# Kernel optimization log

Measured on AMD Instinct MI355X. Metric: run time of the kernel, lower is better.

The kernel has to match this reference:

```python
import jax, jax.numpy as jnp
import numpy as np
import math

B, S, D, H, F = 2, 2048, 1024, 16, 4096
HD = D // H

def _xavier(key, fan_in, fan_out):
    limit = math.sqrt(6.0 / (fan_in + fan_out))
    return jax.random.uniform(key, (fan_in, fan_out), jnp.float32, -limit, limit)

def setup_inputs() -> dict:
    key = jax.random.key(0)
    ks = jax.random.split(key, 8)
    inp = {
        'x': jax.random.normal(ks[0], (B, S, D), jnp.float32),
        # attention projections (stored [in, out]; biases zero-init per module)
        'Wq': _xavier(ks[1], D, D), 'bq': jnp.zeros((D,), jnp.float32),
        'Wk': _xavier(ks[2], D, D), 'bk': jnp.zeros((D,), jnp.float32),
        'Wv': _xavier(ks[3], D, D), 'bv': jnp.zeros((D,), jnp.float32),
        'Wp': _xavier(ks[4], D, D), 'bp': jnp.zeros((D,), jnp.float32),
        # layer norms
        'g1': jnp.ones((D,), jnp.float32), 'be1': jnp.zeros((D,), jnp.float32),
        'g2': jnp.ones((D,), jnp.float32), 'be2': jnp.zeros((D,), jnp.float32),
        # feed-forward
        'W1': _xavier(ks[5], D, F), 'bf1': jnp.zeros((F,), jnp.float32),
        'W2': _xavier(ks[6], F, D), 'bf2': jnp.zeros((D,), jnp.float32),
    }
    return inp

def _layernorm(x, g, b, eps=1e-5):
    mu = jnp.mean(x, axis=-1, keepdims=True)
    var = jnp.var(x, axis=-1, keepdims=True)
    return (x - mu) * jax.lax.rsqrt(var + eps) * g + b

def _block(x, Wq, bq, Wk, bk, Wv, bv, Wp, bp, g1, be1, g2, be2, W1, bf1, W2, bf2):
    b, s, d = x.shape
    # --- pre-LN attention ---
    a_in = _layernorm(x, g1, be1)
    q = (a_in @ Wq + bq).reshape(b, s, H, HD).transpose(0, 2, 1, 3)  # [B,H,S,HD]
    k = (a_in @ Wk + bk).reshape(b, s, H, HD).transpose(0, 2, 1, 3)
    v = (a_in @ Wv + bv).reshape(b, s, H, HD).transpose(0, 2, 1, 3)
    scores = jnp.einsum('bhqd,bhkd->bhqk', q, k) / math.sqrt(HD)
    causal = jnp.tril(jnp.ones((s, s), dtype=bool))
    scores = jnp.where(causal, scores, -jnp.inf)
    attn = jax.nn.softmax(scores, axis=-1)
    out = jnp.einsum('bhqk,bhkd->bhqd', attn, v)
    out = out.transpose(0, 2, 1, 3).reshape(b, s, d)
    x = x + (out @ Wp + bp)
    # --- pre-LN feed-forward ---
    f_in = _layernorm(x, g2, be2)
    h = jax.nn.gelu(f_in @ W1 + bf1, approximate=False)
    x = x + (h @ W2 + bf2)
    return x

def reference(x, Wq, bq, Wk, bk, Wv, bv, Wp, bp, g1, be1, g2, be2, W1, bf1, W2, bf2):
    return _block(x, Wq, bq, Wk, bk, Wv, bv, Wp, bp, g1, be1, g2, be2, W1, bf1, W2, bf2)
```

## Files before the change

### kernel.cpp

```cpp
#include <hip/hip_runtime.h>
#include <hip/hip_bf16.h>

#define AS1 __attribute__((address_space(1)))
#define AS3 __attribute__((address_space(3)))

typedef __bf16 bf16;
typedef __attribute__((ext_vector_type(8))) __bf16 bf16x8;
typedef __attribute__((ext_vector_type(4))) __bf16 bf16x4;
typedef __attribute__((ext_vector_type(4))) float f32x4;

#define NB 2
#define NS 2048
#define ND 1024
#define NH 16
#define NF 4096
#define NHD 64
#define NM (NB*NS)

__device__ __forceinline__ void gload16(const void* g, void* l) {
  __builtin_amdgcn_global_load_lds((AS1 void*)g, (AS3 void*)l, 16, 0, 0);
}

__global__ void tb_wtrans(const float* __restrict__ W, bf16* __restrict__ Wt,
                          int K, int N) {
  __shared__ float t[64][65];
  const int nb = blockIdx.x << 6, kb = blockIdx.y << 6;
  const int tid = threadIdx.x;
#pragma unroll
  for (int i = 0; i < 16; ++i) {
    const int lin = tid + (i << 8);
    const int r = lin >> 6, c = lin & 63;
    t[r][c] = W[(size_t)(kb + r) * N + nb + c];
  }
  __syncthreads();
#pragma unroll
  for (int i = 0; i < 16; ++i) {
    const int lin = tid + (i << 8);
    const int r = lin >> 6, c = lin & 63;
    Wt[(size_t)(nb + r) * K + kb + c] = (bf16)t[c][r];
  }
}

__global__ void tb_vtrans(const bf16* __restrict__ v, bf16* __restrict__ vt) {
  __shared__ bf16 t[64][72];
  const int bh = blockIdx.y;
  const int sb = blockIdx.x << 6;
  const int tid = threadIdx.x;
  const bf16* src = v + ((size_t)bh * NS + sb) * NHD;
  bf16* dst = vt + (size_t)bh * NHD * NS + sb;
  const int r = tid >> 3;
  const int c8 = (tid & 7) << 3;
#pragma unroll
  for (int i = 0; i < 2; ++i) {
    const int row = r + i * 32;
    const bf16x8 xv = *(const bf16x8*)(src + (size_t)row * NHD + c8);
#pragma unroll
    for (int j = 0; j < 8; ++j) t[row][c8 + j] = xv[j];
  }
  __syncthreads();
#pragma unroll
  for (int i = 0; i < 2; ++i) {
    const int row = r + i * 32;
    bf16x8 ov;
#pragma unroll
    for (int j = 0; j < 8; ++j) ov[j] = t[c8 + j][row];
    *(bf16x8*)(dst + (size_t)row * NS + c8) = ov;
  }
}

__global__ void tb_lnorm(const float* __restrict__ xin, const float* __restrict__ g,
                         const float* __restrict__ be, bf16* __restrict__ outp) {
  const int row = blockIdx.x;
  const int tid = threadIdx.x;
  const float4 v = ((const float4*)(xin + (size_t)row * ND))[tid];
  float s  = v.x + v.y + v.z + v.w;
  float ss = v.x*v.x + v.y*v.y + v.z*v.z + v.w*v.w;
#pragma unroll
  for (int off = 32; off; off >>= 1) {
    s  += __shfl_xor(s,  off, 64);
    ss += __shfl_xor(ss, off, 64);
  }
  __shared__ float red[8];
  const int lane = tid & 63, wv = tid >> 6;
  if (lane == 0) { red[wv] = s; red[4 + wv] = ss; }
  __syncthreads();
  s  = red[0] + red[1] + red[2] + red[3];
  ss = red[4] + red[5] + red[6] + red[7];
  const float mu = s * (1.0f / ND);
  const float var = ss * (1.0f / ND) - mu * mu;
  const float rstd = rsqrtf(var + 1e-5f);
  const float4 gv = ((const float4*)g)[tid];
  const float4 bv = ((const float4*)be)[tid];
  bf16x4 o;
  o[0] = (bf16)((v.x - mu) * rstd * gv.x + bv.x);
  o[1] = (bf16)((v.y - mu) * rstd * gv.y + bv.y);
  o[2] = (bf16)((v.z - mu) * rstd * gv.z + bv.z);
  o[3] = (bf16)((v.w - mu) * rstd * gv.w + bv.w);
  ((bf16x4*)(outp + (size_t)row * ND))[tid] = o;
}

template <int MODE>
__global__ void __launch_bounds__(256, 2)
tb_gemm(const bf16* __restrict__ A,
        const bf16* __restrict__ B0, const bf16* __restrict__ B1, const bf16* __restrict__ B2,
        const float* __restrict__ bias0, const float* __restrict__ bias1, const float* __restrict__ bias2,
        const float* __restrict__ resid,
        void* __restrict__ o0, void* __restrict__ o1, void* __restrict__ o2,
        int Ktot) {
  __shared__ __align__(16) bf16 As[128 * 64];
  __shared__ __align__(16) bf16 Bs[128 * 64];
  const bf16* Bt = B0; const float* bias = bias0; void* outp = o0;
  if (MODE == 0) {
    if (blockIdx.z == 1)      { Bt = B1; bias = bias1; outp = o1; }
    else if (blockIdx.z == 2) { Bt = B2; bias = bias2; outp = o2; }
  }
  const int tid = threadIdx.x;
  const int lane = tid & 63, wv = tid >> 6;
  const int wr = wv >> 1, wc = wv & 1;
  const int m0 = blockIdx.y * 128, n0 = blockIdx.x * 128;

  f32x4 acc[4][4] = {};

  const int srow = (wv << 3) + (lane >> 3);
  const int scb  = ((lane & 7) << 4);

  for (int k0 = 0; k0 < Ktot; k0 += 64) {
    __syncthreads();
#pragma unroll
    for (int i = 0; i < 4; ++i) {
      const int row = i * 32 + srow;
      const int cb = scb ^ ((row & 7) << 4);
      gload16(A  + (size_t)(m0 + row) * Ktot + k0 + (cb >> 1), (char*)As + i * 4096 + wv * 1024);
      gload16(Bt + (size_t)(n0 + row) * Ktot + k0 + (cb >> 1), (char*)Bs + i * 4096 + wv * 1024);
    }
    __syncthreads();
#pragma unroll
    for (int kk = 0; kk < 2; ++kk) {
      bf16x8 af[4], bfr[4];
#pragma unroll
      for (int mi = 0; mi < 4; ++mi) {
        const int row = wr * 64 + mi * 16 + (lane & 15);
        const int cb = (kk * 64 + ((lane >> 4) << 4)) ^ ((row & 7) << 4);
        af[mi] = *(const bf16x8*)((const char*)As + row * 128 + cb);
      }
#pragma unroll
      for (int ni = 0; ni < 4; ++ni) {
        const int row = wc * 64 + ni * 16 + (lane & 15);
        const int cb = (kk * 64 + ((lane >> 4) << 4)) ^ ((row & 7) << 4);
        bfr[ni] = *(const bf16x8*)((const char*)Bs + row * 128 + cb);
      }
#pragma unroll
      for (int mi = 0; mi < 4; ++mi)
#pragma unroll
        for (int ni = 0; ni < 4; ++ni)
          acc[mi][ni] = __builtin_amdgcn_mfma_f32_16x16x32_bf16(af[mi], bfr[ni], acc[mi][ni], 0, 0, 0);
    }
  }
#pragma unroll
  for (int mi = 0; mi < 4; ++mi) {
#pragma unroll
    for (int ni = 0; ni < 4; ++ni) {
      const int rbase = m0 + wr * 64 + mi * 16 + ((lane >> 4) << 2);
      const int gcol  = n0 + wc * 64 + ni * 16 + (lane & 15);
#pragma unroll
      for (int r = 0; r < 4; ++r) {
        const int grow = rbase + r;
        const float val = acc[mi][ni][r] + bias[gcol];
        if (MODE == 0) {
          const int b = grow >> 11, sIdx = grow & 2047;
          const int h = gcol >> 6, hd = gcol & 63;
          ((bf16*)outp)[(((size_t)(b * NH + h)) * NS + sIdx) * NHD + hd] = (bf16)val;
        } else if (MODE == 1) {
          const size_t idx = (size_t)grow * ND + gcol;
          ((float*)outp)[idx] = resid[idx] + val;
        } else {
          const float gelu = 0.5f * val * (1.0f + erff(val * 0.70710678f));
          ((bf16*)outp)[(size_t)grow * NF + gcol] = (bf16)gelu;
        }
      }
    }
  }
}

__global__ void __launch_bounds__(256, 4)
tb_attn(const bf16* __restrict__ qg, const bf16* __restrict__ kg,
        const bf16* __restrict__ vtg, bf16* __restrict__ og) {
  __shared__ __align__(16) bf16 Ks[2][64 * 64];
  __shared__ __align__(16) bf16 Vts[2][64 * 64];
  __shared__ __align__(16) bf16 Ps[4][16 * 64];
  const int bid = blockIdx.x;
  const int u = bid & 255, v = bid >> 8;
  const int bh = u & 31;
  const int s = ((u >> 5) << 2) + v;
  const int qt = (s & 1) ? (31 - (s >> 1)) : (s >> 1);
  const int tid = threadIdx.x;
  const int lane = tid & 63, wv = tid >> 6;
  const bf16* Qp  = qg  + (size_t)bh * NS * NHD;
  const bf16* Kp  = kg  + (size_t)bh * NS * NHD;
  const bf16* Vtp = vtg + (size_t)bh * NHD * NS;
  char* const Pw = (char*)&Ps[wv][0];
  const int qbase = qt * 64 + wv * 16;

  bf16x8 qa[2];
#pragma unroll
  for (int kk = 0; kk < 2; ++kk)
    qa[kk] = *(const bf16x8*)(Qp + (size_t)(qbase + (lane & 15)) * NHD
                              + kk * 32 + ((lane >> 4) << 3));

  f32x4 Of[4] = {};
  float mrow[4], lrow[4];
#pragma unroll
  for (int r = 0; r < 4; ++r) { mrow[r] = -1e30f; lrow[r] = 0.0f; }

  const int srow = (wv << 3) + (lane >> 3);
  const int scb  = (lane & 7) << 4;
  const int nkb = qt + 1;

#define STAGE_KV(buf, kbi_) do {                                               \
    _Pragma("unroll")                                                          \
    for (int i_ = 0; i_ < 2; ++i_) {                                           \
      const int row_ = i_ * 32 + srow;                                         \
      const int cb_ = scb ^ ((row_ & 7) << 4);                                 \
      gload16(Kp  + (size_t)((kbi_) * 64 + row_) * NHD + (cb_ >> 1),           \
              (char*)Ks[buf] + i_ * 4096 + wv * 1024);                         \
      gload16(Vtp + (size_t)row_ * NS + (kbi_) * 64 + (cb_ >> 1),              \
              (char*)Vts[buf] + i_ * 4096 + wv * 1024);                        \
    } } while (0)

  STAGE_KV(0, 0);
  __syncthreads();

  for (int kbi = 0; kbi < nkb; ++kbi) {
    const int cur = kbi & 1;
    if (kbi + 1 < nkb) STAGE_KV(cur ^ 1, kbi + 1);
    const bool maskedT = (kbi == qt);

    f32x4 sf[4] = {};
#pragma unroll
    for (int kk = 0; kk < 2; ++kk) {
#pragma unroll
      for (int f = 0; f < 4; ++f) {
        const int row = f * 16 + (lane & 15);
        const int cb = (kk * 64 + ((lane >> 4) << 4)) ^ ((row & 7) << 4);
        const bf16x8 kf = *(const bf16x8*)((const char*)Ks[cur] + row * 128 + cb);
        sf[f] = __builtin_amdgcn_mfma_f32_16x16x32_bf16(qa[kk], kf, sf[f], 0, 0, 0);
      }
    }

    float tmax[4];
#pragma unroll
    for (int r = 0; r < 4; ++r) tmax[r] = -1e30f;
#pragma unroll
    for (int f = 0; f < 4; ++f)
#pragma unroll
      for (int r = 0; r < 4; ++r) {
        float sv = sf[f][r] * 0.125f;
        if (maskedT) {
          const int kcol = kbi * 64 + f * 16 + (lane & 15);
          const int qrow = qbase + ((lane >> 4) << 2) + r;
          sv = (kcol <= qrow) ? sv : -1e30f;
        }
        sf[f][r] = sv;
        tmax[r] = fmaxf(tmax[r], sv);
      }
#pragma unroll
    for (int off = 8; off; off >>= 1)
#pragma unroll
      for (int r = 0; r < 4; ++r)
        tmax[r] = fmaxf(tmax[r], __shfl_xor(tmax[r], off, 64));
#pragma unroll
    for (int r = 0; r < 4; ++r) {
      const float mnew = fmaxf(mrow[r], tmax[r]);
      const float alpha = __expf(mrow[r] - mnew);
      mrow[r] = mnew;
      float ps = 0.0f;
#pragma unroll
      for (int f = 0; f < 4; ++f) {
        const float p = __expf(sf[f][r] - mnew);
        sf[f][r] = p;
        ps += p;
      }
      lrow[r] = lrow[r] * alpha + ps;
#pragma unroll
      for (int hf = 0; hf < 4; ++hf) Of[hf][r] *= alpha;
    }

#pragma unroll
    for (int f = 0; f < 4; ++f) {
      const int col = f * 16 + (lane & 15);
#pragma unroll
      for (int r = 0; r < 4; ++r) {
        const int prow = ((lane >> 4) << 2) + r;
        *(bf16*)(Pw + prow * 128 + ((col * 2) ^ ((prow & 7) << 4))) = (bf16)sf[f][r];
      }
    }

#pragma unroll
    for (int kk = 0; kk < 2; ++kk) {
      const int prow = lane & 15;
      const int pcb = (kk * 64 + ((lane >> 4) << 4)) ^ ((prow & 7) << 4);
      const bf16x8 pa = *(const bf16x8*)(Pw + prow * 128 + pcb);
#pragma unroll
      for (int hf = 0; hf < 4; ++hf) {
        const int vrow = hf * 16 + (lane & 15);
        const int vcb = (kk * 64 + ((lane >> 4) << 4)) ^ ((vrow & 7) << 4);
        const bf16x8 vbf = *(const bf16x8*)((const char*)Vts[cur] + vrow * 128 + vcb);
        Of[hf] = __builtin_amdgcn_mfma_f32_16x16x32_bf16(pa, vbf, Of[hf], 0, 0, 0);
      }
    }
    __syncthreads();
  }
#undef STAGE_KV

#pragma unroll
  for (int off = 8; off; off >>= 1)
#pragma unroll
    for (int r = 0; r < 4; ++r)
      lrow[r] += __shfl_xor(lrow[r], off, 64);
  const int b = bh >> 4, h = bh & 15;
#pragma unroll
  for (int r = 0; r < 4; ++r) {
    const float inv = 1.0f / lrow[r];
    const int q = qbase + ((lane >> 4) << 2) + r;
    bf16* dst = og + ((size_t)b * NS + q) * ND + h * NHD;
#pragma unroll
    for (int hf = 0; hf < 4; ++hf)
      dst[hf * 16 + (lane & 15)] = (bf16)(Of[hf][r] * inv);
  }
}

extern "C" void kernel_launch(void* const* d_in, const int* in_sizes, int n_in,
                              void* d_out, int out_size, void* d_ws, size_t ws_size,
                              hipStream_t stream) {
  (void)in_sizes; (void)n_in; (void)out_size; (void)ws_size;
  const float* x   = (const float*)d_in[0];
  const float* Wq  = (const float*)d_in[1];
  const float* bq  = (const float*)d_in[2];
  const float* Wk  = (const float*)d_in[3];
  const float* bk  = (const float*)d_in[4];
  const float* Wv  = (const float*)d_in[5];
  const float* bv  = (const float*)d_in[6];
  const float* Wp  = (const float*)d_in[7];
  const float* bp  = (const float*)d_in[8];
  const float* g1  = (const float*)d_in[9];
  const float* be1 = (const float*)d_in[10];
  const float* g2  = (const float*)d_in[11];
  const float* be2 = (const float*)d_in[12];
  const float* W1  = (const float*)d_in[13];
  const float* bf1 = (const float*)d_in[14];
  const float* W2  = (const float*)d_in[15];
  const float* bf2 = (const float*)d_in[16];
  float* outp = (float*)d_out;

  char* w = (char*)d_ws;
  bf16* WqT  = (bf16*)(w + (0u  << 20));
  bf16* WkT  = (bf16*)(w + (2u  << 20));
  bf16* WvT  = (bf16*)(w + (4u  << 20));
  bf16* WpT  = (bf16*)(w + (6u  << 20));
  bf16* W1T  = (bf16*)(w + (8u  << 20));
  bf16* W2T  = (bf16*)(w + (16u << 20));
  bf16* Abuf = (bf16*)(w + (24u << 20));
  bf16* vt   = (bf16*)(w + (24u << 20));
  bf16* qb   = (bf16*)(w + (32u << 20));
  bf16* kb   = (bf16*)(w + (40u << 20));
  bf16* vb   = (bf16*)(w + (48u << 20));
  bf16* ao   = (bf16*)(w + (56u << 20));
  bf16* hb   = (bf16*)(w + (32u << 20));
  float* x2  = outp;

  tb_wtrans<<<dim3(16, 16), 256, 0, stream>>>(Wq, WqT, ND, ND);
  tb_wtrans<<<dim3(16, 16), 256, 0, stream>>>(Wk, WkT, ND, ND);
  tb_wtrans<<<dim3(16, 16), 256, 0, stream>>>(Wv, WvT, ND, ND);
  tb_wtrans<<<dim3(16, 16), 256, 0, stream>>>(Wp, WpT, ND, ND);
  tb_wtrans<<<dim3(64, 16), 256, 0, stream>>>(W1, W1T, ND, NF);
  tb_wtrans<<<dim3(16, 64), 256, 0, stream>>>(W2, W2T, NF, ND);

  tb_lnorm<<<NM, 256, 0, stream>>>(x, g1, be1, Abuf);
  tb_gemm<0><<<dim3(8, 32, 3), 256, 0, stream>>>(Abuf, WqT, WkT, WvT, bq, bk, bv,
                                                 nullptr, qb, kb, vb, ND);
  tb_vtrans<<<dim3(32, 32), 256, 0, stream>>>(vb, vt);
  tb_attn<<<1024, 256, 0, stream>>>(qb, kb, vt, ao);
  tb_gemm<1><<<dim3(8, 32, 1), 256, 0, stream>>>(ao, WpT, WpT, WpT, bp, bp, bp,
                                                 x, x2, x2, x2, ND);
  tb_lnorm<<<NM, 256, 0, stream>>>(x2, g2, be2, Abuf);
  tb_gemm<2><<<dim3(32, 32, 1), 256, 0, stream>>>(Abuf, W1T, W1T, W1T, bf1, bf1, bf1,
                                                  nullptr, hb, hb, hb, ND);
  tb_gemm<1><<<dim3(8, 32, 1), 256, 0, stream>>>(hb, W2T, W2T, W2T, bf2, bf2, bf2,
                                                 x2, outp, outp, outp, NF);
}
```

Measured before the change: 280.8 us.

## Multi-buffer GEMM LDS tiles to overlap global loads with MFMA compute

Converts the GEMM main loop from single-buffered load-then-compute into a double- or triple-buffered software pipeline. Tiles for later k-steps are issued with global_load_lds while the current tile is consumed, and explicit vmcnt waits plus s_barrier replace the paired syncthreads. The QKV and FFN1 GEMMs use two buffers; the 256-block output projection and FFN2 GEMMs use three buffers with launch bounds lowered to one block per CU. This aims to hide global memory latency behind MFMA work, at the cost of more LDS per block and possibly lower occupancy.

```diff
diff --git a/kernel.cpp b/kernel.cpp
--- a/kernel.cpp
+++ b/kernel.cpp
@@ -99,16 +99,16 @@
   ((bf16x4*)(outp + (size_t)row * ND))[tid] = o;
 }
 
-template <int MODE>
-__global__ void __launch_bounds__(256, 2)
+template <int MODE, int NBUF>
+__global__ void __launch_bounds__(256, NBUF == 2 ? 2 : 1)
 tb_gemm(const bf16* __restrict__ A,
         const bf16* __restrict__ B0, const bf16* __restrict__ B1, const bf16* __restrict__ B2,
         const float* __restrict__ bias0, const float* __restrict__ bias1, const float* __restrict__ bias2,
         const float* __restrict__ resid,
         void* __restrict__ o0, void* __restrict__ o1, void* __restrict__ o2,
         int Ktot) {
-  __shared__ __align__(16) bf16 As[128 * 64];
-  __shared__ __align__(16) bf16 Bs[128 * 64];
+  __shared__ __align__(16) bf16 As[NBUF * 128 * 64];
+  __shared__ __align__(16) bf16 Bs[NBUF * 128 * 64];
   const bf16* Bt = B0; const float* bias = bias0; void* outp = o0;
   if (MODE == 0) {
     if (blockIdx.z == 1)      { Bt = B1; bias = bias1; outp = o1; }
@@ -123,17 +123,37 @@
 
   const int srow = (wv << 3) + (lane >> 3);
   const int scb  = ((lane & 7) << 4);
-
-  for (int k0 = 0; k0 < Ktot; k0 += 64) {
-    __syncthreads();
-#pragma unroll
-    for (int i = 0; i < 4; ++i) {
-      const int row = i * 32 + srow;
-      const int cb = scb ^ ((row & 7) << 4);
-      gload16(A  + (size_t)(m0 + row) * Ktot + k0 + (cb >> 1), (char*)As + i * 4096 + wv * 1024);
-      gload16(Bt + (size_t)(n0 + row) * Ktot + k0 + (cb >> 1), (char*)Bs + i * 4096 + wv * 1024);
-    }
-    __syncthreads();
+  const int NT = Ktot >> 6;
+
+#define GSTAGE(buf, t_) do {                                                   \
+    _Pragma("unroll")                                                          \
+    for (int i_ = 0; i_ < 4; ++i_) {                                           \
+      const int row_ = i_ * 32 + srow;                                         \
+      const int cb_ = scb ^ ((row_ & 7) << 4);                                 \
+      gload16(A  + (size_t)(m0 + row_) * Ktot + ((t_) << 6) + (cb_ >> 1),      \
+              (char*)As + (buf) * 16384 + i_ * 4096 + wv * 1024);              \
+      gload16(Bt + (size_t)(n0 + row_) * Ktot + ((t_) << 6) + (cb_ >> 1),      \
+              (char*)Bs + (buf) * 16384 + i_ * 4096 + wv * 1024);              \
+    } } while (0)
+
+  GSTAGE(0, 0);
+  if (NBUF == 3 && NT > 1) {
+    GSTAGE(1, 1);
+    asm volatile("s_waitcnt vmcnt(8)" ::: "memory");
+  } else {
+    asm volatile("s_waitcnt vmcnt(0)" ::: "memory");
+  }
+  __builtin_amdgcn_s_barrier();
+
+  int cur = 0;
+  for (int t = 0; t < NT; ++t) {
+    if (NBUF == 2) {
+      if (t + 1 < NT) GSTAGE(cur ^ 1, t + 1);
+    } else {
+      if (t + 2 < NT) GSTAGE((cur + 2 >= 3 ? cur - 1 : cur + 2), t + 2);
+    }
+    const char* Ab = (const char*)As + cur * 16384;
+    const char* Bb = (const char*)Bs + cur * 16384;
 #pragma unroll
     for (int kk = 0; kk < 2; ++kk) {
       bf16x8 af[4], bfr[4];
@@ -141,13 +161,13 @@
       for (int mi = 0; mi < 4; ++mi) {
         const int row = wr * 64 + mi * 16 + (lane & 15);
         const int cb = (kk * 64 + ((lane >> 4) << 4)) ^ ((row & 7) << 4);
-        af[mi] = *(const bf16x8*)((const char*)As + row * 128 + cb);
+        af[mi] = *(const bf16x8*)(Ab + row * 128 + cb);
       }
 #pragma unroll
       for (int ni = 0; ni < 4; ++ni) {
         const int row = wc * 64 + ni * 16 + (lane & 15);
         const int cb = (kk * 64 + ((lane >> 4) << 4)) ^ ((row & 7) << 4);
-        bfr[ni] = *(const bf16x8*)((const char*)Bs + row * 128 + cb);
+        bfr[ni] = *(const bf16x8*)(Bb + row * 128 + cb);
       }
 #pragma unroll
       for (int mi = 0; mi < 4; ++mi)
@@ -155,7 +175,17 @@
         for (int ni = 0; ni < 4; ++ni)
           acc[mi][ni] = __builtin_amdgcn_mfma_f32_16x16x32_bf16(af[mi], bfr[ni], acc[mi][ni], 0, 0, 0);
     }
-  }
+    if (t + 1 < NT) {
+      if (NBUF == 3 && t + 2 < NT)
+        asm volatile("s_waitcnt vmcnt(8)" ::: "memory");
+      else
+        asm volatile("s_waitcnt vmcnt(0)" ::: "memory");
+      __builtin_amdgcn_s_barrier();
+    }
+    cur = (cur + 1 == NBUF) ? 0 : cur + 1;
+  }
+#undef GSTAGE
+
 #pragma unroll
   for (int mi = 0; mi < 4; ++mi) {
 #pragma unroll
@@ -376,15 +406,15 @@
   tb_wtrans<<<dim3(16, 64), 256, 0, stream>>>(W2, W2T, NF, ND);
 
   tb_lnorm<<<NM, 256, 0, stream>>>(x, g1, be1, Abuf);
-  tb_gemm<0><<<dim3(8, 32, 3), 256, 0, stream>>>(Abuf, WqT, WkT, WvT, bq, bk, bv,
-                                                 nullptr, qb, kb, vb, ND);
+  tb_gemm<0, 2><<<dim3(8, 32, 3), 256, 0, stream>>>(Abuf, WqT, WkT, WvT, bq, bk, bv,
+                                                    nullptr, qb, kb, vb, ND);
   tb_vtrans<<<dim3(32, 32), 256, 0, stream>>>(vb, vt);
   tb_attn<<<1024, 256, 0, stream>>>(qb, kb, vt, ao);
-  tb_gemm<1><<<dim3(8, 32, 1), 256, 0, stream>>>(ao, WpT, WpT, WpT, bp, bp, bp,
-                                                 x, x2, x2, x2, ND);
+  tb_gemm<1, 3><<<dim3(8, 32, 1), 256, 0, stream>>>(ao, WpT, WpT, WpT, bp, bp, bp,
+                                                    x, x2, x2, x2, ND);
   tb_lnorm<<<NM, 256, 0, stream>>>(x2, g2, be2, Abuf);
-  tb_gemm<2><<<dim3(32, 32, 1), 256, 0, stream>>>(Abuf, W1T, W1T, W1T, bf1, bf1, bf1,
-                                                  nullptr, hb, hb, hb, ND);
-  tb_gemm<1><<<dim3(8, 32, 1), 256, 0, stream>>>(hb, W2T, W2T, W2T, bf2, bf2, bf2,
-                                                 x2, outp, outp, outp, NF);
-}
+  tb_gemm<2, 2><<<dim3(32, 32, 1), 256, 0, stream>>>(Abuf, W1T, W1T, W1T, bf1, bf1, bf1,
+                                                     nullptr, hb, hb, hb, ND);
+  tb_gemm<1, 3><<<dim3(8, 32, 1), 256, 0, stream>>>(hb, W2T, W2T, W2T, bf2, bf2, bf2,
+                                                    x2, outp, outp, outp, NF);
+}
```

Result: slower. 292.7 us (+4.3%).

## Use 64x128 double-buffered GEMM tiles for the two N=1024 residual projections

Applied to the files above, without the earlier changes.

Adds a tb_gemm64 kernel with 64-row by 128-column tiles and double-buffered LDS staging, so the next K tile loads while the current one is multiplied. It replaces the MODE 1 path for the attention output projection and the FFN down projection. Both GEMMs have N=1024, so 128x128 tiles launched only 256 blocks. The smaller M tile doubles that to 512 blocks to fill the CUs better. The cost is less operand reuse per block, and the extra LDS buffer may lower occupancy.

```diff
diff --git a/kernel.cpp b/kernel.cpp
--- a/kernel.cpp
+++ b/kernel.cpp
@@ -104,7 +104,6 @@
 tb_gemm(const bf16* __restrict__ A,
         const bf16* __restrict__ B0, const bf16* __restrict__ B1, const bf16* __restrict__ B2,
         const float* __restrict__ bias0, const float* __restrict__ bias1, const float* __restrict__ bias2,
-        const float* __restrict__ resid,
         void* __restrict__ o0, void* __restrict__ o1, void* __restrict__ o2,
         int Ktot) {
   __shared__ __align__(16) bf16 As[128 * 64];
@@ -170,13 +169,95 @@
           const int b = grow >> 11, sIdx = grow & 2047;
           const int h = gcol >> 6, hd = gcol & 63;
           ((bf16*)outp)[(((size_t)(b * NH + h)) * NS + sIdx) * NHD + hd] = (bf16)val;
-        } else if (MODE == 1) {
-          const size_t idx = (size_t)grow * ND + gcol;
-          ((float*)outp)[idx] = resid[idx] + val;
         } else {
           const float gelu = 0.5f * val * (1.0f + erff(val * 0.70710678f));
           ((bf16*)outp)[(size_t)grow * NF + gcol] = (bf16)gelu;
         }
+      }
+    }
+  }
+}
+
+__global__ void __launch_bounds__(256, 2)
+tb_gemm64(const bf16* __restrict__ A, const bf16* __restrict__ Bt,
+          const float* __restrict__ bias, const float* __restrict__ resid,
+          float* __restrict__ outp, int Ktot) {
+  __shared__ __align__(16) bf16 As[2][64 * 64];
+  __shared__ __align__(16) bf16 Bs[2][128 * 64];
+  const int tid = threadIdx.x;
+  const int lane = tid & 63, wv = tid >> 6;
+  const int wr = wv >> 1, wc = wv & 1;
+  const int m0 = blockIdx.y * 64, n0 = blockIdx.x * 128;
+
+  f32x4 acc[2][4] = {};
+
+  const int srow = (wv << 3) + (lane >> 3);
+  const int scb  = ((lane & 7) << 4);
+  const int NT = Ktot >> 6;
+
+#define GSTAGE64(buf, t_) do {                                                 \
+    _Pragma("unroll")                                                          \
+    for (int i_ = 0; i_ < 2; ++i_) {                                           \
+      const int row_ = i_ * 32 + srow;                                         \
+      const int cb_ = scb ^ ((row_ & 7) << 4);                                 \
+      gload16(A + (size_t)(m0 + row_) * Ktot + ((t_) << 6) + (cb_ >> 1),       \
+              (char*)As[buf] + i_ * 4096 + wv * 1024);                         \
+    }                                                                          \
+    _Pragma("unroll")                                                          \
+    for (int i_ = 0; i_ < 4; ++i_) {                                           \
+      const int row_ = i_ * 32 + srow;                                         \
+      const int cb_ = scb ^ ((row_ & 7) << 4);                                 \
+      gload16(Bt + (size_t)(n0 + row_) * Ktot + ((t_) << 6) + (cb_ >> 1),      \
+              (char*)Bs[buf] + i_ * 4096 + wv * 1024);                         \
+    } } while (0)
+
+  GSTAGE64(0, 0);
+  asm volatile("s_waitcnt vmcnt(0)" ::: "memory");
+  __builtin_amdgcn_s_barrier();
+
+  for (int t = 0; t < NT; ++t) {
+    const int cur = t & 1;
+    if (t + 1 < NT) GSTAGE64(cur ^ 1, t + 1);
+    const char* Ab = (const char*)As[cur];
+    const char* Bb = (const char*)Bs[cur];
+#pragma unroll
+    for (int kk = 0; kk < 2; ++kk) {
+      bf16x8 af[2], bfr[4];
+#pragma unroll
+      for (int mi = 0; mi < 2; ++mi) {
+        const int row = wr * 32 + mi * 16 + (lane & 15);
+        const int cb = (kk * 64 + ((lane >> 4) << 4)) ^ ((row & 7) << 4);
+        af[mi] = *(const bf16x8*)(Ab + row * 128 + cb);
+      }
+#pragma unroll
+      for (int ni = 0; ni < 4; ++ni) {
+        const int row = wc * 64 + ni * 16 + (lane & 15);
+        const int cb = (kk * 64 + ((lane >> 4) << 4)) ^ ((row & 7) << 4);
+        bfr[ni] = *(const bf16x8*)(Bb + row * 128 + cb);
+      }
+#pragma unroll
+      for (int mi = 0; mi < 2; ++mi)
+#pragma unroll
+        for (int ni = 0; ni < 4; ++ni)
+          acc[mi][ni] = __builtin_amdgcn_mfma_f32_16x16x32_bf16(af[mi], bfr[ni], acc[mi][ni], 0, 0, 0);
+    }
+    if (t + 1 < NT) {
+      asm volatile("s_waitcnt vmcnt(0)" ::: "memory");
+      __builtin_amdgcn_s_barrier();
+    }
+  }
+#undef GSTAGE64
+
+#pragma unroll
+  for (int mi = 0; mi < 2; ++mi) {
+#pragma unroll
+    for (int ni = 0; ni < 4; ++ni) {
+      const int rbase = m0 + wr * 32 + mi * 16 + ((lane >> 4) << 2);
+      const int gcol  = n0 + wc * 64 + ni * 16 + (lane & 15);
+#pragma unroll
+      for (int r = 0; r < 4; ++r) {
+        const size_t idx = (size_t)(rbase + r) * ND + gcol;
+        outp[idx] = resid[idx] + acc[mi][ni][r] + bias[gcol];
       }
     }
   }
@@ -377,14 +458,12 @@
 
   tb_lnorm<<<NM, 256, 0, stream>>>(x, g1, be1, Abuf);
   tb_gemm<0><<<dim3(8, 32, 3), 256, 0, stream>>>(Abuf, WqT, WkT, WvT, bq, bk, bv,
-                                                 nullptr, qb, kb, vb, ND);
+                                                 qb, kb, vb, ND);
   tb_vtrans<<<dim3(32, 32), 256, 0, stream>>>(vb, vt);
   tb_attn<<<1024, 256, 0, stream>>>(qb, kb, vt, ao);
-  tb_gemm<1><<<dim3(8, 32, 1), 256, 0, stream>>>(ao, WpT, WpT, WpT, bp, bp, bp,
-                                                 x, x2, x2, x2, ND);
+  tb_gemm64<<<dim3(8, 64), 256, 0, stream>>>(ao, WpT, bp, x, x2, ND);
   tb_lnorm<<<NM, 256, 0, stream>>>(x2, g2, be2, Abuf);
   tb_gemm<2><<<dim3(32, 32, 1), 256, 0, stream>>>(Abuf, W1T, W1T, W1T, bf1, bf1, bf1,
-                                                  nullptr, hb, hb, hb, ND);
-  tb_gemm<1><<<dim3(8, 32, 1), 256, 0, stream>>>(hb, W2T, W2T, W2T, bf2, bf2, bf2,
-                                                 x2, outp, outp, outp, NF);
-}
+                                                  hb, hb, hb, ND);
+  tb_gemm64<<<dim3(8, 64), 256, 0, stream>>>(hb, W2T, bf2, x2, outp, NF);
+}
```

New measurement: 266.5 us. 5.1% less time.
